# Performance work log

Measured on AMD Instinct MI355X. Metric: run time of the kernel, lower is better.

## Reference

```python
import jax, jax.numpy as jnp
import numpy as np

N_HEAD = 16
ROPE_BASE = 10000.0
EPS = 1e-6


def _rms_norm(x):
    return x / jnp.sqrt(jnp.mean(x * x, axis=-1, keepdims=True) + EPS)


def _rotary_cos_sin(n_pos, dim, dtype):
    # NOTE: faithful to the source, n_pos == n_head (not seq_len) because
    # Rotary.forward reads x.shape[2] of a (B,T,H,D) tensor.
    inv_freq = 1.0 / (ROPE_BASE ** (jnp.arange(0, dim, 2, dtype=jnp.float32) / dim))
    t = jnp.arange(n_pos, dtype=jnp.float32)
    freqs = jnp.outer(t, inv_freq)  # (n_pos, dim//2)
    return jnp.cos(freqs).astype(dtype)[None, None], jnp.sin(freqs).astype(dtype)[None, None]


def _apply_rotary(x, cos, sin):
    d = x.shape[-1] // 2
    x1, x2 = x[..., :d], x[..., d:]
    return jnp.concatenate([x1 * cos + x2 * sin, -x1 * sin + x2 * cos], axis=-1)


def setup_inputs() -> dict:
    key = jax.random.key(0)
    ks = jax.random.split(key, 8)
    B, T, C = 4, 1024, 2048
    x = jax.random.normal(ks[0], (B, T, C), dtype=jnp.float32)
    v1 = jax.random.normal(ks[1], (B, T, N_HEAD, C // N_HEAD), dtype=jnp.float32)
    s = 0.02
    W_qkv = jax.random.normal(ks[2], (C, 3 * C), dtype=jnp.float32) * s
    b_qkv = jax.random.normal(ks[3], (3 * C,), dtype=jnp.float32) * s
    W_proj = jax.random.normal(ks[4], (C, C), dtype=jnp.float32) * s
    b_proj = jax.random.normal(ks[5], (C,), dtype=jnp.float32) * s
    lamb = jnp.float32(0.5)
    return {"x": x, "v1": v1, "W_qkv": W_qkv, "b_qkv": b_qkv,
            "W_proj": W_proj, "b_proj": b_proj, "lamb": lamb}


def reference(x, v1, W_qkv, b_qkv, W_proj, b_proj, lamb):
    B, T, C = x.shape
    H = N_HEAD
    D = C // H
    qkv = x @ W_qkv + b_qkv  # (B,T,3C)
    q, k, v = jnp.split(qkv, 3, axis=-1)
    q = q.reshape(B, T, H, D)
    k = k.reshape(B, T, H, D)
    v = v.reshape(B, T, H, D)
    v1 = v1.reshape(B, T, H, D)
    value = (1.0 - lamb) * v + lamb * v1  # lambda value-residual mix
    q = _rms_norm(q)
    k = _rms_norm(k)
    cos, sin = _rotary_cos_sin(H, D, x.dtype)  # rotary over head axis (source bug, kept)
    q = _apply_rotary(q, cos, sin)
    k = _apply_rotary(k, cos, sin)
    # causal attention, default flex_attention scale 1/sqrt(D)
    scale = 1.0 / jnp.sqrt(jnp.float32(D)).astype(x.dtype)
    scores = jnp.einsum('bqhd,bkhd->bhqk', q, k) * scale
    causal = jnp.tril(jnp.ones((T, T), dtype=bool))
    scores = jnp.where(causal[None, None], scores, jnp.finfo(scores.dtype).min)
    probs = jax.nn.softmax(scores, axis=-1)
    attn = jnp.einsum('bhqk,bkhd->bqhd', probs, value).reshape(B, T, C)
    out = attn @ W_proj + b_proj
    return out, v1
```

## Files before the change

kernel.cpp:

```cpp
#include <hip/hip_runtime.h>
#include <stdint.h>
#include <stddef.h>

typedef unsigned short u16;
typedef __attribute__((ext_vector_type(8))) short  bf16x8;
typedef __attribute__((ext_vector_type(4))) unsigned short u16x4;
typedef __attribute__((ext_vector_type(4))) float  f32x4;

#define DEVI __device__ __forceinline__

DEVI float bf2f(u16 u){ union{uint32_t i; float f;} v; v.i = ((uint32_t)u)<<16; return v.f; }
DEVI u16 f2bf(float f){ union{float f; uint32_t i;} v; v.f=f; uint32_t r = v.i + 0x7fffu + ((v.i>>16)&1u); return (u16)(r>>16); }

DEVI void gload_lds16(const void* g, void* l){
  __builtin_amdgcn_global_load_lds((const __attribute__((address_space(1))) void*)g,
                                   (__attribute__((address_space(3))) void*)l, 16, 0, 0);
}

__global__ __launch_bounds__(256) void k_prep(
    const float* __restrict__ x,     u16* __restrict__ xb,
    const float* __restrict__ Wqkv,  u16* __restrict__ WqkvT,
    const float* __restrict__ Wproj, u16* __restrict__ WprojT)
{
  __shared__ float tile[32][33];
  int bid = blockIdx.x;
  int tid = threadIdx.x;
  if (bid < 2048){
    int i = (bid*256 + tid)*4;
    const int st = 2048*256*4;
    for (; i < 8388608; i += st){
      f32x4 v = *(const f32x4*)(x + i);
      u16x4 o;
      #pragma unroll
      for (int j=0;j<4;j++) o[j] = f2bf(v[j]);
      *(u16x4*)(xb + i) = o;
    }
    return;
  }
  const float* in; u16* out; int K, N, nb, kb;
  if (bid < 2048 + 12288){
    int b2 = bid - 2048; in = Wqkv; out = WqkvT; K = 2048; N = 6144;
    nb = (b2 % 192)*32; kb = (b2 / 192)*32;
  } else {
    int b3 = bid - 2048 - 12288; in = Wproj; out = WprojT; K = 2048; N = 2048;
    nb = (b3 % 64)*32; kb = (b3 / 64)*32;
  }
  int tx = tid & 31, ty = tid >> 5;
  #pragma unroll
  for (int i=0;i<32;i+=8)
    tile[ty+i][tx] = in[(size_t)(kb+ty+i)*N + nb+tx];
  __syncthreads();
  #pragma unroll
  for (int i=0;i<32;i+=8)
    out[(size_t)(nb+ty+i)*K + kb+tx] = f2bf(tile[tx][ty+i]);
}

#define STG_A(SLAB, GSRC) \
  gload_lds16((GSRC) + off0, (SLAB) + tid*8);
#define STG_B(SLAB, GSRC) \
  gload_lds16((GSRC) + off0, (SLAB) + tid*8); \
  gload_lds16((GSRC) + off1, (SLAB) + 4096 + tid*8);

#define RD4(SLAB, ROWBASE, DST) \
  { _Pragma("unroll") for (int f=0; f<4; f++){ \
      int row_ = (ROWBASE) + f*16 + lr; \
      int rp_ = row_>>1; \
      int slot_ = ((((row_&1)<<2) | lg) ^ (rp_&7)); \
      DST[f] = *(const bf16x8*)((const char*)(SLAB) + rp_*128 + slot_*16); } }

#define MM16(AA, BB) \
  __builtin_amdgcn_s_setprio(1); \
  { _Pragma("unroll") for (int f=0; f<4; f++) \
    { _Pragma("unroll") for (int nf=0; nf<4; nf++) \
      acc[f][nf] = __builtin_amdgcn_mfma_f32_16x16x32_bf16(AA[f], BB[nf], acc[f][nf], 0,0,0); } } \
  __builtin_amdgcn_s_setprio(0);

#define BAR_LGKM \
  __builtin_amdgcn_s_barrier(); \
  __builtin_amdgcn_sched_barrier(0); \
  asm volatile("s_waitcnt lgkmcnt(0)" ::: "memory"); \
  __builtin_amdgcn_sched_barrier(0);

#define WAITV(N) asm volatile("s_waitcnt vmcnt(" #N ")" ::: "memory");
#define ORDER_FENCE __builtin_amdgcn_sched_barrier(0); asm volatile("" ::: "memory");

template<bool OUT_BF16>
__global__ __launch_bounds__(512) void k_gemm128x256(
    const u16* __restrict__ A, const u16* __restrict__ Bt,
    const float* __restrict__ bias, void* __restrict__ Cout,
    int M, int N, int K, int nbnx)
{
  __shared__ __attribute__((aligned(16))) u16 sA[3][2][4096];
  __shared__ __attribute__((aligned(16))) u16 sB[3][2][8192];
  int orig = blockIdx.x;
  int xcd = orig & 7;
  int idx = orig >> 3;
  int bnx = idx % nbnx;
  int bm  = idx / nbnx;
  int bn  = xcd*nbnx + bnx;
  const int tid = threadIdx.x;
  const int wid = tid>>6, l = tid&63;
  const int lr = l&15, lg = l>>4;
  const int wm = wid>>2, wn = wid&3;
  const int rba = wm*64, rbb = wn*64;

  uint32_t off0, off1;
  { int cc=tid;     int rp=cc>>3, cb=(cc&7)^(rp&7); off0 = (uint32_t)((rp*2+(cb>>2))*K + (cb&3)*8); }
  { int cc=512+tid; int rp=cc>>3, cb=(cc&7)^(rp&7); off1 = (uint32_t)((rp*2+(cb>>2))*K + (cb&3)*8); }
  const u16* Ab = A + (size_t)bm*128*K;
  const u16* Bb = Bt + (size_t)bn*256*K;

  f32x4 acc[4][4] = {};
  bf16x8 a0[4], a1[4], b0[4], b1[4];
  const int NT = K>>6;

  STG_B(&sB[0][0][0], Bb);      STG_A(&sA[0][0][0], Ab);      ORDER_FENCE;
  STG_B(&sB[0][1][0], Bb+32);   STG_A(&sA[0][1][0], Ab+32);   ORDER_FENCE;
  STG_B(&sB[1][0][0], Bb+64);   STG_A(&sA[1][0][0], Ab+64);
  WAITV(6);
  __builtin_amdgcn_s_barrier();
  __builtin_amdgcn_sched_barrier(0);

  int s0=0, s1=1, s2=2;
  for (int t=0; t<=NT-3; ++t){
    const u16* A1 = Ab + (t+1)*64;  const u16* B1 = Bb + (t+1)*64;
    const u16* A2 = Ab + (t+2)*64;  const u16* B2 = Bb + (t+2)*64;
    RD4(&sB[s0][0][0], rbb, b0); RD4(&sA[s0][0][0], rba, a0);
    STG_B(&sB[s1][1][0], B1+32); STG_A(&sA[s1][1][0], A1+32);
    WAITV(6);
    BAR_LGKM; MM16(a0, b0);
    RD4(&sB[s0][1][0], rbb, b1); RD4(&sA[s0][1][0], rba, a1);
    STG_B(&sB[s2][0][0], B2);    STG_A(&sA[s2][0][0], A2);
    WAITV(6);
    BAR_LGKM; MM16(a1, b1);
    int tmp=s0; s0=s1; s1=s2; s2=tmp;
  }
  {
    const u16* A1 = Ab + (NT-1)*64;  const u16* B1 = Bb + (NT-1)*64;
    RD4(&sB[s0][0][0], rbb, b0); RD4(&sA[s0][0][0], rba, a0);
    STG_B(&sB[s1][1][0], B1+32); STG_A(&sA[s1][1][0], A1+32);
    WAITV(6);
    BAR_LGKM; MM16(a0, b0);
    RD4(&sB[s0][1][0], rbb, b1); RD4(&sA[s0][1][0], rba, a1);
    WAITV(3);
    BAR_LGKM; MM16(a1, b1);
  }
  {
    RD4(&sB[s1][0][0], rbb, b0); RD4(&sA[s1][0][0], rba, a0);
    WAITV(0);
    BAR_LGKM; MM16(a0, b0);
    RD4(&sB[s1][1][0], rbb, b1); RD4(&sA[s1][1][0], rba, a1);
    BAR_LGKM; MM16(a1, b1);
  }

  #pragma unroll
  for (int nf=0; nf<4; nf++){
    int col = bn*256 + wn*64 + nf*16 + lr;
    float bv = bias[col];
    #pragma unroll
    for (int m=0; m<4; m++){
      #pragma unroll
      for (int j=0; j<4; j++){
        int row = bm*128 + wm*64 + m*16 + lg*4 + j;
        float v = acc[m][nf][j] + bv;
        if (OUT_BF16) ((u16*)Cout)[(size_t)row*N + col] = f2bf(v);
        else          ((float*)Cout)[(size_t)row*N + col] = v;
      }
    }
  }
}

DEVI void unpack16(const u16* p, float* f){
  bf16x8 a = *(const bf16x8*)p, b = *(const bf16x8*)(p+8);
  #pragma unroll
  for (int i=0;i<8;i++){ f[i]=bf2f((u16)a[i]); f[8+i]=bf2f((u16)b[i]); }
}

__global__ __launch_bounds__(256) void k_qkv_post(
    const u16*  __restrict__ qkv,
    const float* __restrict__ v1,
    const float* __restrict__ lambp,
    u16* __restrict__ qn,
    u16* __restrict__ kn,
    u16* __restrict__ vT,
    float* __restrict__ v1out)
{
  __shared__ float cosv[64], sinv[64];
  __shared__ __attribute__((aligned(16))) u16 sv[64][136];
  int bid = blockIdx.x;
  int tb = bid & 15, h = (bid>>4)&15, b = bid>>8;
  int tid = threadIdx.x;
  if (tid < 64){
    float ang = (float)h * exp2f(-(float)tid * 0.2076205059304595f);
    cosv[tid] = cosf(ang);
    sinv[tid] = sinf(ang);
  }
  float lamb = lambp[0];
  int row = tid>>2, p = tid&3;
  int t = tb*64 + row;
  size_t base = ((size_t)(b*1024 + t))*6144 + (size_t)h*128;
  __syncthreads();

  #pragma unroll
  for (int qc=0; qc<2; ++qc){
    const u16* src = qkv + base + qc*2048;
    u16* dst = (qc==0 ? qn : kn) + ((size_t)(b*1024+t))*2048 + h*128;
    int j0 = p*16;
    float x1[16], x2[16];
    unpack16(src + j0, x1);
    unpack16(src + 64 + j0, x2);
    float ss = 0.f;
    #pragma unroll
    for (int i=0;i<16;i++) ss += x1[i]*x1[i] + x2[i]*x2[i];
    ss += __shfl_xor(ss, 1);
    ss += __shfl_xor(ss, 2);
    float rn = rsqrtf(ss*(1.0f/128.0f) + 1e-6f);
    bf16x8 o1a,o1b,o2a,o2b;
    #pragma unroll
    for (int i=0;i<16;i++){
      float c = cosv[j0+i], s = sinv[j0+i];
      u16 a = f2bf(( x1[i]*c + x2[i]*s)*rn);
      u16 bq= f2bf((-x1[i]*s + x2[i]*c)*rn);
      if (i<8){ o1a[i]=(short)a; o2a[i]=(short)bq; } else { o1b[i-8]=(short)a; o2b[i-8]=(short)bq; }
    }
    *(bf16x8*)(dst + j0)      = o1a;
    *(bf16x8*)(dst + j0 + 8)  = o1b;
    *(bf16x8*)(dst + 64 + j0)     = o2a;
    *(bf16x8*)(dst + 64 + j0 + 8) = o2b;
  }

  {
    const u16* srcv = qkv + base + 4096;
    size_t v1off = (((size_t)(b*1024+t))*16 + h)*128;
    const float* src1 = v1 + v1off;
    float* dst1 = v1out + v1off;
    int d0 = p*32;
    #pragma unroll
    for (int c8=0;c8<4;c8++){
      bf16x8 vv = *(const bf16x8*)(srcv + d0 + c8*8);
      f32x4 a0 = *(const f32x4*)(src1 + d0 + c8*8);
      f32x4 a1 = *(const f32x4*)(src1 + d0 + c8*8 + 4);
      *(f32x4*)(dst1 + d0 + c8*8) = a0;
      *(f32x4*)(dst1 + d0 + c8*8 + 4) = a1;
      bf16x8 o;
      #pragma unroll
      for (int i=0;i<8;i++){
        float x1v = (i<4)? a0[i] : a1[i-4];
        o[i] = (short)f2bf((1.0f-lamb)*bf2f((u16)vv[i]) + lamb*x1v);
      }
      *(bf16x8*)(&sv[row][d0 + c8*8]) = o;
    }
  }
  __syncthreads();
  {
    int d = tid>>1, tc = (tid&1)*32;
    u16 tmp[32];
    #pragma unroll
    for (int i=0;i<32;i++) tmp[i] = sv[tc+i][d];
    u16* dst = vT + (((size_t)(b*16+h))*128 + d)*1024 + tb*64 + tc;
    #pragma unroll
    for (int c8=0;c8<4;c8++){
      bf16x8 o;
      #pragma unroll
      for (int i=0;i<8;i++) o[i]=(short)tmp[c8*8+i];
      *(bf16x8*)(dst + c8*8) = o;
    }
  }
}

__global__ __launch_bounds__(256) void k_attn(
    const u16* __restrict__ Q,
    const u16* __restrict__ Kn,
    const u16* __restrict__ Vt,
    u16* __restrict__ O)
{
  __shared__ __attribute__((aligned(16))) u16 sK[2][64*128];
  __shared__ __attribute__((aligned(16))) u16 sV[2][128*64];
  __shared__ __attribute__((aligned(16))) u16 sP[4][16*64];
  int bid = blockIdx.x;
  int qi = 15 - (bid>>6);
  int bh = bid & 63;
  int h = bh & 15, b = bh >> 4;
  int tid = threadIdx.x, w = tid>>6, l = tid&63, lr = l&15, lg = l>>4;
  int qrow = qi*64 + w*16;
  bf16x8 aq[4];
  {
    const u16* qp = Q + ((size_t)(b*1024 + qrow + lr))*2048 + h*128 + lg*8;
    #pragma unroll
    for (int ks=0; ks<4; ++ks) aq[ks] = *(const bf16x8*)(qp + ks*32);
  }
  f32x4 accO[8] = {};
  float mrun[4], srun[4];
  #pragma unroll
  for (int j=0;j<4;j++){ mrun[j] = -INFINITY; srun[j]=0.f; }
  const float scale = 0.08838834764831845f;
  const size_t kbase = (size_t)(b*1024)*2048 + (size_t)h*128;
  const u16* vbase = Vt + ((size_t)(b*16+h))*128*1024;

  auto STAGE = [&](int kt, int buf){
    #pragma unroll
    for (int it=0; it<4; ++it){
      int c = it*256+tid;
      int key = c>>4, d16 = (c&15)^(key&7);
      gload_lds16(Kn + kbase + (size_t)(kt*64+key)*2048 + d16*8, &sK[buf][c*8]);
    }
    #pragma unroll
    for (int it=0; it<4; ++it){
      int c = it*256+tid;
      int d = c>>3, k8 = (c&7)^(d&7);
      gload_lds16(vbase + (size_t)d*1024 + kt*64 + k8*8, &sV[buf][c*8]);
    }
  };

  STAGE(0, 0);
  int cur = 0;
  for (int kt=0; kt<=qi; ++kt){
    if (kt < qi){
      STAGE(kt+1, cur^1);
      asm volatile("s_waitcnt vmcnt(8)" ::: "memory");
    } else {
      asm volatile("s_waitcnt vmcnt(0)" ::: "memory");
    }
    __builtin_amdgcn_s_barrier();
    __builtin_amdgcn_sched_barrier(0);
    const char* kb = (const char*)sK[cur];
    const char* vb = (const char*)sV[cur];

    f32x4 accS[4] = {};
    __builtin_amdgcn_s_setprio(1);
    #pragma unroll
    for (int ks=0; ks<4; ++ks){
      #pragma unroll
      for (int n=0;n<4;n++){
        int key = n*16+lr, k = ks*32+lg*8;
        int byt = ((key<<8) + (k<<1)) ^ ((key&7)<<4);
        bf16x8 bk = *(const bf16x8*)(kb + byt);
        accS[n] = __builtin_amdgcn_mfma_f32_16x16x32_bf16(aq[ks], bk, accS[n], 0,0,0);
      }
    }
    __builtin_amdgcn_s_setprio(0);
    bool diag = (kt == qi);
    float pj[4][4];
    #pragma unroll
    for (int j=0;j<4;j++){
      int qg = qrow + lg*4 + j;
      float mx = -INFINITY;
      #pragma unroll
      for (int n=0;n<4;n++){
        float s = accS[n][j]*scale;
        if (diag && (kt*64 + n*16 + lr) > qg) s = -1e30f;
        pj[n][j] = s;
        mx = fmaxf(mx, s);
      }
      #pragma unroll
      for (int off=1; off<16; off<<=1) mx = fmaxf(mx, __shfl_xor(mx, off));
      float mnew = fmaxf(mrun[j], mx);
      float fac = __expf(mrun[j] - mnew);
      float ps = 0.f;
      #pragma unroll
      for (int n=0;n<4;n++){ float e = __expf(pj[n][j]-mnew); pj[n][j]=e; ps += e; }
      #pragma unroll
      for (int off=1; off<16; off<<=1) ps += __shfl_xor(ps, off);
      srun[j] = srun[j]*fac + ps;
      mrun[j] = mnew;
      #pragma unroll
      for (int n=0;n<8;n++) accO[n][j] *= fac;
    }
    #pragma unroll
    for (int n=0;n<4;n++)
      #pragma unroll
      for (int j=0;j<4;j++){
        int q = lg*4+j, key = n*16+lr;
        int byt = ((q<<7) + (key<<1)) ^ ((q&7)<<4);
        *(u16*)((char*)sP[w] + byt) = f2bf(pj[n][j]);
      }
    bf16x8 pA[2];
    #pragma unroll
    for (int ks=0; ks<2; ++ks){
      int k = ks*32 + lg*8;
      int byt = ((lr<<7) + (k<<1)) ^ ((lr&7)<<4);
      pA[ks] = *(const bf16x8*)((const char*)sP[w] + byt);
    }
    __builtin_amdgcn_s_setprio(1);
    #pragma unroll
    for (int ks=0; ks<2; ++ks)
      #pragma unroll
      for (int n=0;n<8;n++){
        int d = n*16+lr, k = ks*32+lg*8;
        int byt = ((d<<7) + (k<<1)) ^ ((d&7)<<4);
        bf16x8 bv = *(const bf16x8*)(vb + byt);
        accO[n] = __builtin_amdgcn_mfma_f32_16x16x32_bf16(pA[ks], bv, accO[n], 0,0,0);
      }
    __builtin_amdgcn_s_setprio(0);
    __builtin_amdgcn_s_barrier();
    cur ^= 1;
  }
  #pragma unroll
  for (int j=0;j<4;j++){
    float inv = 1.0f / srun[j];
    int row = qrow + lg*4 + j;
    u16* op = O + ((size_t)(b*1024+row))*2048 + h*128;
    #pragma unroll
    for (int n=0;n<8;n++)
      op[n*16+lr] = f2bf(accO[n][j]*inv);
  }
}

extern "C" void kernel_launch(void* const* d_in, const int* in_sizes, int n_in,
                              void* d_out, int out_size, void* d_ws, size_t ws_size,
                              hipStream_t stream)
{
  const float* x     = (const float*)d_in[0];
  const float* v1    = (const float*)d_in[1];
  const float* Wqkv  = (const float*)d_in[2];
  const float* bqkv  = (const float*)d_in[3];
  const float* Wproj = (const float*)d_in[4];
  const float* bproj = (const float*)d_in[5];
  const float* lamb  = (const float*)d_in[6];

  char* ws = (char*)d_ws;
  u16* qkv_b  = (u16*)(ws);
  u16* WqkvT  = (u16*)(ws +  50331648);
  u16* WprojT = (u16*)(ws +  75497472);
  u16* xb     = (u16*)(ws +  83886080);
  u16* vT     = xb;
  u16* qn     = (u16*)(ws + 100663296);
  u16* kn     = (u16*)(ws + 117440512);
  u16* attn_b = qkv_b;

  float* out = (float*)d_out;

  hipLaunchKernelGGL(k_prep, dim3(2048+12288+4096), dim3(256), 0, stream,
                     x, xb, Wqkv, WqkvT, Wproj, WprojT);
  hipLaunchKernelGGL((k_gemm128x256<true>),  dim3(768), dim3(512), 0, stream, xb, WqkvT, bqkv, (void*)qkv_b, 4096, 6144, 2048, 3);
  hipLaunchKernelGGL(k_qkv_post, dim3(1024), dim3(256), 0, stream, qkv_b, v1, lamb, qn, kn, vT, out + 8388608);
  hipLaunchKernelGGL(k_attn, dim3(1024), dim3(256), 0, stream, qn, kn, vT, attn_b);
  hipLaunchKernelGGL((k_gemm128x256<false>), dim3(256), dim3(512), 0, stream, attn_b, WprojT, bproj, (void*)out, 4096, 2048, 2048, 1);
}
```

Baseline: 273.1 us.

## Restructure GEMM to 4 waves with 128x64 per-wave tiles and 2 blocks/CU

Rewrites the shared bf16 GEMM kernel to use 256 threads (4 waves), each computing a full 128x64 output strip with 8x4 MFMA accumulators. The K loop now steps 32 at a time through a 3-slot LDS ring, prefetching one step ahead with a single barrier per step. LDS use is halved, so launch bounds request 2 blocks per CU. The goal is a better ratio of LDS fragment reads to MFMAs and higher occupancy. The trade-offs are shallower prefetch, a barrier every 32-wide K step, and higher register pressure from the larger accumulator set.

```diff
diff --git a/kernel.cpp b/kernel.cpp
--- a/kernel.cpp
+++ b/kernel.cpp
@@ -55,114 +55,103 @@
     out[(size_t)(nb+ty+i)*K + kb+tx] = f2bf(tile[tx][ty+i]);
 }
 
-#define STG_A(SLAB, GSRC) \
-  gload_lds16((GSRC) + off0, (SLAB) + tid*8);
-#define STG_B(SLAB, GSRC) \
-  gload_lds16((GSRC) + off0, (SLAB) + tid*8); \
-  gload_lds16((GSRC) + off1, (SLAB) + 4096 + tid*8);
-
-#define RD4(SLAB, ROWBASE, DST) \
-  { _Pragma("unroll") for (int f=0; f<4; f++){ \
-      int row_ = (ROWBASE) + f*16 + lr; \
+#define NSTG(SLOT, T) \
+  { const u16* As_ = Ab + (T)*32; const u16* Bs_ = Bb + (T)*32; \
+    gload_lds16(As_ + offA[0], &sA[SLOT][0] + tid*8); \
+    gload_lds16(As_ + offA[1], &sA[SLOT][0] + 2048 + tid*8); \
+    gload_lds16(Bs_ + offB[0], &sB[SLOT][0] + tid*8); \
+    gload_lds16(Bs_ + offB[1], &sB[SLOT][0] + 2048 + tid*8); \
+    gload_lds16(Bs_ + offB[2], &sB[SLOT][0] + 4096 + tid*8); \
+    gload_lds16(Bs_ + offB[3], &sB[SLOT][0] + 6144 + tid*8); }
+
+#define NRD_A(SLAB) \
+  { _Pragma("unroll") for (int f=0; f<8; f++){ \
+      int row_ = f*16 + lr; \
       int rp_ = row_>>1; \
       int slot_ = ((((row_&1)<<2) | lg) ^ (rp_&7)); \
-      DST[f] = *(const bf16x8*)((const char*)(SLAB) + rp_*128 + slot_*16); } }
-
-#define MM16(AA, BB) \
-  __builtin_amdgcn_s_setprio(1); \
-  { _Pragma("unroll") for (int f=0; f<4; f++) \
-    { _Pragma("unroll") for (int nf=0; nf<4; nf++) \
-      acc[f][nf] = __builtin_amdgcn_mfma_f32_16x16x32_bf16(AA[f], BB[nf], acc[f][nf], 0,0,0); } } \
-  __builtin_amdgcn_s_setprio(0);
-
-#define BAR_LGKM \
-  __builtin_amdgcn_s_barrier(); \
-  __builtin_amdgcn_sched_barrier(0); \
-  asm volatile("s_waitcnt lgkmcnt(0)" ::: "memory"); \
-  __builtin_amdgcn_sched_barrier(0);
+      af[f] = *(const bf16x8*)((const char*)(SLAB) + rp_*128 + slot_*16); } }
+
+#define NRD_B(SLAB) \
+  { _Pragma("unroll") for (int nf=0; nf<4; nf++){ \
+      int row_ = wid*64 + nf*16 + lr; \
+      int rp_ = row_>>1; \
+      int slot_ = ((((row_&1)<<2) | lg) ^ (rp_&7)); \
+      bfr[nf] = *(const bf16x8*)((const char*)(SLAB) + rp_*128 + slot_*16); } }
 
 #define WAITV(N) asm volatile("s_waitcnt vmcnt(" #N ")" ::: "memory");
 #define ORDER_FENCE __builtin_amdgcn_sched_barrier(0); asm volatile("" ::: "memory");
 
 template<bool OUT_BF16>
-__global__ __launch_bounds__(512) void k_gemm128x256(
+__global__ __launch_bounds__(256, 2) void k_gemm128x256(
     const u16* __restrict__ A, const u16* __restrict__ Bt,
     const float* __restrict__ bias, void* __restrict__ Cout,
     int M, int N, int K, int nbnx)
 {
-  __shared__ __attribute__((aligned(16))) u16 sA[3][2][4096];
-  __shared__ __attribute__((aligned(16))) u16 sB[3][2][8192];
+  __shared__ __attribute__((aligned(16))) u16 sA[3][4096];
+  __shared__ __attribute__((aligned(16))) u16 sB[3][8192];
   int orig = blockIdx.x;
   int xcd = orig & 7;
   int idx = orig >> 3;
-  int bnx = idx % nbnx;
+  int bn  = xcd*nbnx + idx % nbnx;
   int bm  = idx / nbnx;
-  int bn  = xcd*nbnx + bnx;
   const int tid = threadIdx.x;
   const int wid = tid>>6, l = tid&63;
   const int lr = l&15, lg = l>>4;
-  const int wm = wid>>2, wn = wid&3;
-  const int rba = wm*64, rbb = wn*64;
-
-  uint32_t off0, off1;
-  { int cc=tid;     int rp=cc>>3, cb=(cc&7)^(rp&7); off0 = (uint32_t)((rp*2+(cb>>2))*K + (cb&3)*8); }
-  { int cc=512+tid; int rp=cc>>3, cb=(cc&7)^(rp&7); off1 = (uint32_t)((rp*2+(cb>>2))*K + (cb&3)*8); }
+
+  uint32_t offA[2], offB[4];
+  #pragma unroll
+  for (int p=0; p<4; p++){
+    int cc = p*256 + tid;
+    int rp = cc>>3, cb = (cc&7)^(rp&7);
+    uint32_t off = (uint32_t)((rp*2 + (cb>>2))*K + (cb&3)*8);
+    offB[p] = off;
+    if (p < 2) offA[p] = off;
+  }
   const u16* Ab = A + (size_t)bm*128*K;
   const u16* Bb = Bt + (size_t)bn*256*K;
 
-  f32x4 acc[4][4] = {};
-  bf16x8 a0[4], a1[4], b0[4], b1[4];
-  const int NT = K>>6;
-
-  STG_B(&sB[0][0][0], Bb);      STG_A(&sA[0][0][0], Ab);      ORDER_FENCE;
-  STG_B(&sB[0][1][0], Bb+32);   STG_A(&sA[0][1][0], Ab+32);   ORDER_FENCE;
-  STG_B(&sB[1][0][0], Bb+64);   STG_A(&sA[1][0][0], Ab+64);
-  WAITV(6);
-  __builtin_amdgcn_s_barrier();
-  __builtin_amdgcn_sched_barrier(0);
-
-  int s0=0, s1=1, s2=2;
-  for (int t=0; t<=NT-3; ++t){
-    const u16* A1 = Ab + (t+1)*64;  const u16* B1 = Bb + (t+1)*64;
-    const u16* A2 = Ab + (t+2)*64;  const u16* B2 = Bb + (t+2)*64;
-    RD4(&sB[s0][0][0], rbb, b0); RD4(&sA[s0][0][0], rba, a0);
-    STG_B(&sB[s1][1][0], B1+32); STG_A(&sA[s1][1][0], A1+32);
-    WAITV(6);
-    BAR_LGKM; MM16(a0, b0);
-    RD4(&sB[s0][1][0], rbb, b1); RD4(&sA[s0][1][0], rba, a1);
-    STG_B(&sB[s2][0][0], B2);    STG_A(&sA[s2][0][0], A2);
-    WAITV(6);
-    BAR_LGKM; MM16(a1, b1);
-    int tmp=s0; s0=s1; s1=s2; s2=tmp;
-  }
-  {
-    const u16* A1 = Ab + (NT-1)*64;  const u16* B1 = Bb + (NT-1)*64;
-    RD4(&sB[s0][0][0], rbb, b0); RD4(&sA[s0][0][0], rba, a0);
-    STG_B(&sB[s1][1][0], B1+32); STG_A(&sA[s1][1][0], A1+32);
-    WAITV(6);
-    BAR_LGKM; MM16(a0, b0);
-    RD4(&sB[s0][1][0], rbb, b1); RD4(&sA[s0][1][0], rba, a1);
-    WAITV(3);
-    BAR_LGKM; MM16(a1, b1);
-  }
-  {
-    RD4(&sB[s1][0][0], rbb, b0); RD4(&sA[s1][0][0], rba, a0);
-    WAITV(0);
-    BAR_LGKM; MM16(a0, b0);
-    RD4(&sB[s1][1][0], rbb, b1); RD4(&sA[s1][1][0], rba, a1);
-    BAR_LGKM; MM16(a1, b1);
+  f32x4 acc[8][4] = {};
+  bf16x8 af[8], bfr[4];
+  const int NT = K>>5;
+
+  NSTG(0, 0);
+  ORDER_FENCE;
+
+  int s0 = 0;
+  for (int t=0; t<NT; ++t){
+    int s1 = (s0==2) ? 0 : s0+1;
+    if (t+1 < NT){
+      NSTG(s1, t+1);
+      WAITV(6);
+    } else {
+      WAITV(0);
+    }
+    __builtin_amdgcn_s_barrier();
+    __builtin_amdgcn_sched_barrier(0);
+    NRD_B(&sB[s0][0]);
+    NRD_A(&sA[s0][0]);
+    asm volatile("s_waitcnt lgkmcnt(0)" ::: "memory");
+    __builtin_amdgcn_sched_barrier(0);
+    __builtin_amdgcn_s_setprio(1);
+    #pragma unroll
+    for (int f=0; f<8; f++)
+      #pragma unroll
+      for (int nf=0; nf<4; nf++)
+        acc[f][nf] = __builtin_amdgcn_mfma_f32_16x16x32_bf16(af[f], bfr[nf], acc[f][nf], 0,0,0);
+    __builtin_amdgcn_s_setprio(0);
+    s0 = s1;
   }
 
   #pragma unroll
   for (int nf=0; nf<4; nf++){
-    int col = bn*256 + wn*64 + nf*16 + lr;
+    int col = bn*256 + wid*64 + nf*16 + lr;
     float bv = bias[col];
     #pragma unroll
-    for (int m=0; m<4; m++){
+    for (int f=0; f<8; f++){
       #pragma unroll
       for (int j=0; j<4; j++){
-        int row = bm*128 + wm*64 + m*16 + lg*4 + j;
-        float v = acc[m][nf][j] + bv;
+        int row = bm*128 + f*16 + lg*4 + j;
+        float v = acc[f][nf][j] + bv;
         if (OUT_BF16) ((u16*)Cout)[(size_t)row*N + col] = f2bf(v);
         else          ((float*)Cout)[(size_t)row*N + col] = v;
       }
@@ -432,8 +421,8 @@
 
   hipLaunchKernelGGL(k_prep, dim3(2048+12288+4096), dim3(256), 0, stream,
                      x, xb, Wqkv, WqkvT, Wproj, WprojT);
-  hipLaunchKernelGGL((k_gemm128x256<true>),  dim3(768), dim3(512), 0, stream, xb, WqkvT, bqkv, (void*)qkv_b, 4096, 6144, 2048, 3);
+  hipLaunchKernelGGL((k_gemm128x256<true>),  dim3(768), dim3(256), 0, stream, xb, WqkvT, bqkv, (void*)qkv_b, 4096, 6144, 2048, 3);
   hipLaunchKernelGGL(k_qkv_post, dim3(1024), dim3(256), 0, stream, qkv_b, v1, lamb, qn, kn, vT, out + 8388608);
   hipLaunchKernelGGL(k_attn, dim3(1024), dim3(256), 0, stream, qn, kn, vT, attn_b);
-  hipLaunchKernelGGL((k_gemm128x256<false>), dim3(256), dim3(512), 0, stream, attn_b, WprojT, bproj, (void*)out, 4096, 2048, 2048, 1);
-}
+  hipLaunchKernelGGL((k_gemm128x256<false>), dim3(256), dim3(256), 0, stream, attn_b, WprojT, bproj, (void*)out, 4096, 2048, 2048, 1);
+}
```

Measured after the change: 292.6 us. +7.1%, slower.
